# Optimization experiments

Measured on AMD Instinct MI355X. Metric: run time of the kernel, lower is better.

## Reference

```python
import jax, jax.numpy as jnp
import numpy as np
from jax import lax

# Dense-equivalent of the spconv net: SubMConv/SparseConv with stride 1 and
# size-preserving padding on a dense input reduce to ordinary conv2d.
# Layer chain: (1->64,k1) PReLU (64->256,k3) PReLU (256->512,k3) PReLU
# (512->256,k3) PReLU (256->64,k3) PReLU (64->1,k3) PReLU, then symmetrize.

CHANS = [(1, 64, 1), (64, 256, 3), (256, 512, 3), (512, 256, 3), (256, 64, 3), (64, 1, 3)]


def _conv(x, w, b, k):
    pad = ((k // 2, k // 2), (k // 2, k // 2))
    y = lax.conv_general_dilated(x, w, window_strides=(1, 1), padding=pad,
                                 dimension_numbers=('NCHW', 'OIHW', 'NCHW'))
    return y + b[None, :, None, None]


def _prelu(x, a):
    return jnp.where(x >= 0, x, a * x)


def setup_inputs() -> dict:
    key = jax.random.key(0)
    keys = jax.random.split(key, 1 + 2 * len(CHANS))
    inp = {'A': jax.random.normal(keys[0], (1, 1, 512, 512), dtype=jnp.float32)}
    for i, (cin, cout, k) in enumerate(CHANS):
        fan_in = cin * k * k
        std = 1.0 / np.sqrt(fan_in)
        inp[f'w{i}'] = jax.random.normal(keys[1 + 2 * i], (cout, cin, k, k), dtype=jnp.float32) * std
        inp[f'b{i}'] = jax.random.normal(keys[2 + 2 * i], (cout,), dtype=jnp.float32) * std
        inp[f'p{i}'] = jnp.full((1,), 0.25, dtype=jnp.float32)  # PReLU default weight
    return inp


def reference(A, w0, b0, p0, w1, b1, p1, w2, b2, p2, w3, b3, p3, w4, b4, p4, w5, b5, p5):
    params = [(w0, b0, p0), (w1, b1, p1), (w2, b2, p2), (w3, b3, p3), (w4, b4, p4), (w5, b5, p5)]
    x = A
    for (w, b, p), (_, _, k) in zip(params, CHANS):
        x = _prelu(_conv(x, w, b, k), p)
    # make_symmetric: average with transpose over the spatial (matrix) dims
    return 0.5 * (x + jnp.swapaxes(x, -1, -2))
```

## Files before the change

### kernel.cpp

```cpp
#include <hip/hip_runtime.h>
#include <hip/hip_bf16.h>
#include <stdint.h>

typedef __bf16 bf16_t;
typedef __bf16 bf16x8 __attribute__((ext_vector_type(8)));
typedef float  f32x4  __attribute__((ext_vector_type(4)));

#define HP 514
#define AS1 __attribute__((address_space(1)))
#define AS3 __attribute__((address_space(3)))

__device__ __forceinline__ bf16_t f2bf(float f) { return (bf16_t)f; }

__global__ void l0_kernel(const float* __restrict__ A, const float* __restrict__ w0,
                          const float* __restrict__ b0, const float* __restrict__ p0,
                          bf16_t* __restrict__ X0)
{
    int idx = blockIdx.x * 256 + threadIdx.x;
    if (idx >= HP * HP * 64) return;
    int c   = idx & 63;
    int pix = idx >> 6;
    int py = pix / HP, px = pix - py * HP;
    float v = 0.f;
    if (py >= 1 && py <= 512 && px >= 1 && px <= 512) {
        float a = A[(py - 1) * 512 + (px - 1)];
        v = fmaf(w0[c], a, b0[c]);
        v = v >= 0.f ? v : p0[0] * v;
    }
    X0[idx] = f2bf(v);
}

__global__ void zero_rows_kernel(bf16_t* __restrict__ buf, int C, int r0, int n)
{
    int idx = blockIdx.x * 256 + threadIdx.x;
    int rowsz = HP * C;
    if (idx >= n * rowsz) return;
    int r = idx / rowsz, j = idx - r * rowsz;
    buf[(size_t)(r0 + r) * rowsz + j] = f2bf(0.f);
}

__global__ void zero_cols_kernel(bf16_t* __restrict__ buf, int C, int R)
{
    int idx = blockIdx.x * 256 + threadIdx.x;
    if (idx >= R * 2 * C) return;
    int r = idx / (2 * C);
    int t = idx - r * 2 * C;
    int col = (t < C) ? 0 : 513;
    int c = t % C;
    buf[((size_t)r * HP + col) * C + c] = f2bf(0.f);
}

__global__ void wtrans_kernel(const float* __restrict__ w, bf16_t* __restrict__ wt,
                              int COUT, int CIN)
{
    int idx = blockIdx.x * 256 + threadIdx.x;
    if (idx >= COUT * CIN * 9) return;
    int G    = COUT / 16;
    int j    = idx & 7;
    int l    = (idx >> 3) & 63;
    int t    = idx >> 9;
    int gabs = t % G;
    int t2   = t / G;
    int tap  = t2 % 9;
    int ci   = t2 / 9;
    int cout = gabs * 16 + (l & 15);
    int cin  = ci * 32 + (l >> 4) * 8 + j;
    wt[idx] = f2bf(w[(cout * CIN + cin) * 9 + tap]);
}

template<int CIN, int COUT, int BN>
__global__ __launch_bounds__(256, 2)
void conv3x3_kernel(const bf16_t* __restrict__ in, const bf16_t* __restrict__ wt,
                    const float* __restrict__ bias, const float* __restrict__ alpha,
                    bf16_t* __restrict__ out,
                    int n_rows, int in_off, int in_alloc, int out_off)
{
    constexpr int G      = COUT / 16;
    constexpr int GPB    = BN / 16;
    constexpr int NT     = BN / 32;
    constexpr int NC     = CIN / 32;
    constexpr int AUNITS = 18 * 10 * 4;
    constexpr int ASLAB  = AUNITS * 8;
    constexpr int BSZ    = BN * 32;
    __shared__ __align__(16) bf16_t As[2 * ASLAB];
    __shared__ __align__(16) bf16_t Bs[2 * BSZ];

    const int tid  = threadIdx.x;
    const int lane = tid & 63;
    const int wave = tid >> 6;
    const int lm   = lane & 15;
    const int quad = lane >> 4;
    const int wave_m = wave >> 1;
    const int wave_n = wave & 1;

    const int x0 = blockIdx.x * 8;
    const int y0 = blockIdx.y * 16;
    const int zb = blockIdx.z;
    const int gb_blk = zb * GPB;

    int a_src[3], a_dst[3];
    #pragma unroll
    for (int it = 0; it < 3; ++it) {
        int u  = it * 256 + tid;
        int uu = u < AUNITS ? u : 0;
        int q = uu & 3, px = (uu >> 2) % 10, r = uu / 40;
        int grow = in_off + y0 + r;
        grow = grow < 0 ? 0 : (grow >= in_alloc ? in_alloc - 1 : grow);
        a_src[it] = (grow * HP + x0 + px) * CIN + q * 8;
        a_dst[it] = (r * 40 + px * 4 + ((q + (px >> 1)) & 3)) * 8;
    }

    const int pxb = lm & 7, pyb = lm >> 3;
    int sw[3];
    #pragma unroll
    for (int dx = 0; dx < 3; ++dx)
        sw[dx] = ((quad + ((pxb + dx) >> 1)) & 3) * 8;
    int addrA0[4];
    #pragma unroll
    for (int mt = 0; mt < 4; ++mt)
        addrA0[mt] = ((wave_m * 8 + mt * 2 + pyb) * 40 + pxb * 4) * 8;

    auto loadA = [&](int cc, bf16x8* s) {
        #pragma unroll
        for (int it = 0; it < 3; ++it)
            if (it * 256 + tid < AUNITS)
                s[it] = *(const bf16x8*)(in + a_src[it] + cc);
    };
    auto writeA = [&](const bf16x8* s, int abuf) {
        bf16_t* d = As + abuf * ASLAB;
        #pragma unroll
        for (int it = 0; it < 3; ++it)
            if (it * 256 + tid < AUNITS)
                *(bf16x8*)(d + a_dst[it]) = s[it];
    };
    auto stageB = [&](int ci9t, int bbuf) {
        #pragma unroll
        for (int k = 0; k < GPB / 4; ++k) {
            int g = wave + k * 4;
            const bf16_t* src = wt + ((size_t)ci9t * G + gb_blk + g) * 512 + lane * 8;
            bf16_t* dst = Bs + bbuf * BSZ + g * 512;
            __builtin_amdgcn_global_load_lds((AS1 void*)src, (AS3 void*)dst, 16, 0, 0);
        }
    };

    f32x4 acc[4][NT] = {};
    bf16x8 areg[3];

    loadA(0, areg);
    writeA(areg, 0);
    stageB(0, 0);
    __syncthreads();

    int ab = 0, bb = 0;
    for (int ci = 0; ci < NC; ++ci) {
        const bool more = (ci + 1 < NC);
        #pragma unroll
        for (int tap = 0; tap < 9; ++tap) {
            if (tap < 8)      stageB(ci * 9 + tap + 1, bb ^ 1);
            else if (more)    stageB((ci + 1) * 9, bb ^ 1);
            if (tap == 0 && more) loadA((ci + 1) * 32, areg);

            const int dy = tap / 3, dx = tap - dy * 3;
            const int shift = (dy * 40 + dx * 4) * 8 + sw[dx];
            bf16x8 a[4], b[NT];
            #pragma unroll
            for (int nt = 0; nt < NT; ++nt)
                b[nt] = *(const bf16x8*)(Bs + bb * BSZ + (wave_n * NT + nt) * 512 + lane * 8);
            #pragma unroll
            for (int mt = 0; mt < 4; ++mt)
                a[mt] = *(const bf16x8*)(As + ab * ASLAB + addrA0[mt] + shift);
            #pragma unroll
            for (int mt = 0; mt < 4; ++mt)
                #pragma unroll
                for (int nt = 0; nt < NT; ++nt)
                    acc[mt][nt] = __builtin_amdgcn_mfma_f32_16x16x32_bf16(
                        a[mt], b[nt], acc[mt][nt], 0, 0, 0);

            if (tap == 8 && more) writeA(areg, ab ^ 1);
            __syncthreads();
            bb ^= 1;
        }
        ab ^= 1;
    }

    const float al = alpha[0];
    #pragma unroll
    for (int nt = 0; nt < NT; ++nt) {
        const int n = zb * BN + wave_n * (BN / 2) + nt * 16 + lm;
        const float bv = bias[n];
        #pragma unroll
        for (int mt = 0; mt < 4; ++mt) {
            f32x4 v = acc[mt][nt];
            #pragma unroll
            for (int r = 0; r < 4; ++r) {
                int m  = wave_m * 64 + mt * 16 + quad * 4 + r;
                int py = m >> 3, px = m & 7;
                int ly = y0 + py;
                if (ly < n_rows) {
                    float f = v[r] + bv;
                    f = f >= 0.f ? f : al * f;
                    out[((size_t)(out_off + ly) * HP + (x0 + px + 1)) * COUT + n] = f2bf(f);
                }
            }
        }
    }
}

__device__ __forceinline__ float conv64_at(const bf16_t* __restrict__ X,
                                           const float* __restrict__ wsh,
                                           int y, int x, float bv)
{
    float acc = bv;
    #pragma unroll
    for (int dy = 0; dy < 3; ++dy) {
        #pragma unroll
        for (int dx = 0; dx < 3; ++dx) {
            const bf16x8* p = (const bf16x8*)(X + ((size_t)(y + dy) * HP + (x + dx)) * 64);
            const float* wf = wsh + (dy * 3 + dx) * 64;
            #pragma unroll
            for (int j = 0; j < 8; ++j) {
                bf16x8 v = p[j];
                #pragma unroll
                for (int k = 0; k < 8; ++k)
                    acc = fmaf((float)v[k], wf[j * 8 + k], acc);
            }
        }
    }
    return acc;
}

__global__ __launch_bounds__(256)
void l5_strip_kernel(const bf16_t* __restrict__ B4, const bf16_t* __restrict__ wt5,
                     const float* __restrict__ b5, const float* __restrict__ p5,
                     float* __restrict__ T, int abs_row0)
{
    __shared__ float wsh[9 * 64];
    for (int i = threadIdx.x; i < 576; i += 256) wsh[i] = (float)wt5[i];
    __syncthreads();
    int idx = blockIdx.x * 256 + threadIdx.x;
    int ly = idx >> 9, x = idx & 511;
    float bv = b5[0], al = p5[0];
    float t = conv64_at(B4, wsh, ly, x, bv);
    t = t >= 0.f ? t : al * t;
    T[(size_t)(abs_row0 + ly) * 512 + x] = t;
}

__global__ void wtrans5_kernel(const float* __restrict__ w, bf16_t* __restrict__ wt)
{
    int idx = blockIdx.x * 256 + threadIdx.x;
    if (idx >= 9 * 64) return;
    int cin = idx % 64, tap = idx / 64;
    wt[idx] = f2bf(w[cin * 9 + tap]);
}

__global__ __launch_bounds__(256)
void sym_kernel(const float* __restrict__ T, float* __restrict__ out)
{
    int idx = blockIdx.x * 256 + threadIdx.x;
    int y = idx >> 9, x = idx & 511;
    out[idx] = 0.5f * (T[idx] + T[x * 512 + y]);
}

extern "C" void kernel_launch(void* const* d_in, const int* in_sizes, int n_in,
                              void* d_out, int out_size, void* d_ws, size_t ws_size,
                              hipStream_t stream)
{
    const float* A = (const float*)d_in[0];
    const float *w[6], *b[6], *p[6];
    for (int i = 0; i < 6; ++i) {
        w[i] = (const float*)d_in[1 + 3 * i];
        b[i] = (const float*)d_in[2 + 3 * i];
        p[i] = (const float*)d_in[3 + 3 * i];
    }

    auto footprint = [](long long S) -> size_t {
        auto al = [](size_t v) { return (v + 255) & ~(size_t)255; };
        size_t t = 0;
        t += al((size_t)HP * HP * 64 * 2);
        t += al((size_t)(S + 8) * HP * 256 * 2);
        t += al((size_t)(S + 6) * HP * 512 * 2);
        t += al((size_t)(S + 2) * HP * 64 * 2);
        t += al((size_t)512 * 512 * 4);
        t += al((size_t)9 * 256 * 64 * 2);
        t += al((size_t)9 * 512 * 256 * 2);
        t += al((size_t)9 * 256 * 512 * 2);
        t += al((size_t)9 * 64 * 256 * 2);
        t += al((size_t)9 * 64 * 2);
        return t;
    };
    const int cand[6] = {512, 256, 128, 64, 32, 16};
    int S = 16;
    for (int i = 0; i < 6; ++i)
        if (footprint(cand[i]) <= ws_size) { S = cand[i]; break; }
    const int nStrips = 512 / S;

    char* ws = (char*)d_ws;
    size_t off = 0;
    auto carve = [&](size_t bytes) -> void* {
        void* r = ws + off;
        off += (bytes + 255) & ~(size_t)255;
        return r;
    };
    bf16_t* X0  = (bf16_t*)carve((size_t)HP * HP * 64 * 2);
    bf16_t* B1  = (bf16_t*)carve((size_t)(S + 8) * HP * 256 * 2);
    bf16_t* B2  = (bf16_t*)carve((size_t)(S + 6) * HP * 512 * 2);
    bf16_t* B4  = (bf16_t*)carve((size_t)(S + 2) * HP * 64 * 2);
    float*  T   = (float*)carve((size_t)512 * 512 * 4);
    bf16_t* wt1 = (bf16_t*)carve((size_t)9 * 256 * 64 * 2);
    bf16_t* wt2 = (bf16_t*)carve((size_t)9 * 512 * 256 * 2);
    bf16_t* wt3 = (bf16_t*)carve((size_t)9 * 256 * 512 * 2);
    bf16_t* wt4 = (bf16_t*)carve((size_t)9 * 64 * 256 * 2);
    bf16_t* wt5 = (bf16_t*)carve((size_t)9 * 64 * 2);
    bf16_t* B3  = B1;

    auto cdiv = [](int a, int bq) { return (a + bq - 1) / bq; };
    auto zrows = [&](bf16_t* buf, int C, int r0, int n) {
        if (n > 0)
            zero_rows_kernel<<<cdiv(n * HP * C, 256), 256, 0, stream>>>(buf, C, r0, n);
    };

    wtrans_kernel<<<cdiv(9 * 256 * 64, 256), 256, 0, stream>>>(w[1], wt1, 256, 64);
    wtrans_kernel<<<cdiv(9 * 512 * 256, 256), 256, 0, stream>>>(w[2], wt2, 512, 256);
    wtrans_kernel<<<cdiv(9 * 256 * 512, 256), 256, 0, stream>>>(w[3], wt3, 256, 512);
    wtrans_kernel<<<cdiv(9 * 64 * 256, 256), 256, 0, stream>>>(w[4], wt4, 64, 256);
    wtrans5_kernel<<<cdiv(9 * 64, 256), 256, 0, stream>>>(w[5], wt5);
    l0_kernel<<<cdiv(HP * HP * 64, 256), 256, 0, stream>>>(A, w[0], b[0], p[0], X0);
    zero_cols_kernel<<<cdiv((S + 8) * 2 * 256, 256), 256, 0, stream>>>(B1, 256, S + 8);
    zero_cols_kernel<<<cdiv((S + 6) * 2 * 512, 256), 256, 0, stream>>>(B2, 512, S + 6);
    zero_cols_kernel<<<cdiv((S + 2) * 2 * 64, 256), 256, 0, stream>>>(B4, 64, S + 2);

    for (int s = 0; s < nStrips; ++s) {
        const int base = S * s;
        int o0[5], nn[5], ooff[5], alloc[5];
        for (int k = 1; k <= 4; ++k) {
            int hk = 5 - k;
            int a0 = base - hk, a1 = base + S + hk;
            int c0 = a0 < 0 ? 0 : a0, c1 = a1 > 512 ? 512 : a1;
            o0[k] = c0; nn[k] = c1 - c0; ooff[k] = c0 - a0; alloc[k] = S + 2 * hk;
        }
        {
            int in_off = o0[1];
            dim3 g(64, cdiv(nn[1], 16), 2);
            conv3x3_kernel<64, 256, 128><<<g, 256, 0, stream>>>(
                X0, wt1, b[1], p[1], B1, nn[1], in_off, 514, ooff[1]);
            zrows(B1, 256, 0, ooff[1]);
            zrows(B1, 256, ooff[1] + nn[1], alloc[1] - ooff[1] - nn[1]);
        }
        {
            int in_off = (o0[2] - 1) - (base - 4);
            dim3 g(64, cdiv(nn[2], 16), 4);
            conv3x3_kernel<256, 512, 128><<<g, 256, 0, stream>>>(
                B1, wt2, b[2], p[2], B2, nn[2], in_off, alloc[1], ooff[2]);
            zrows(B2, 512, 0, ooff[2]);
            zrows(B2, 512, ooff[2] + nn[2], alloc[2] - ooff[2] - nn[2]);
        }
        {
            int in_off = (o0[3] - 1) - (base - 3);
            dim3 g(64, cdiv(nn[3], 16), 2);
            conv3x3_kernel<512, 256, 128><<<g, 256, 0, stream>>>(
                B2, wt3, b[3], p[3], B3, nn[3], in_off, alloc[2], ooff[3]);
            zrows(B3, 256, 0, ooff[3]);
            zrows(B3, 256, ooff[3] + nn[3], alloc[3] - ooff[3] - nn[3]);
        }
        {
            int in_off = (o0[4] - 1) - (base - 2);
            dim3 g(64, cdiv(nn[4], 16), 1);
            conv3x3_kernel<256, 64, 64><<<g, 256, 0, stream>>>(
                B3, wt4, b[4], p[4], B4, nn[4], in_off, alloc[3], ooff[4]);
            zrows(B4, 64, 0, ooff[4]);
            zrows(B4, 64, ooff[4] + nn[4], alloc[4] - ooff[4] - nn[4]);
        }
        l5_strip_kernel<<<(S * 512) / 256, 256, 0, stream>>>(B4, wt5, b[5], p[5], T, base);
    }

    sym_kernel<<<(512 * 512) / 256, 256, 0, stream>>>(T, (float*)d_out);
}
```

Before: 1.680 ms.

## Enlarge conv3x3 spatial tile to 16x16 and flatten grid with cout-fastest ordering

Doubles each block's spatial tile from 16x8 to 16x16 pixels, so each wave now computes 8 M-tiles instead of 4. The input halo overhead per output pixel drops and each B-fragment load feeds twice as many MFMAs. The 3D grid becomes a 1D grid in which the cout-block index varies fastest, so blocks sharing the same input tile run close together and can reuse it through the cache. In exchange the accumulators double (8xNT f32x4) and LDS use grows, which raises register pressure and may cut occupancy under launch_bounds(256,2).

```diff
diff --git a/kernel.cpp b/kernel.cpp
--- a/kernel.cpp
+++ b/kernel.cpp
@@ -77,10 +77,12 @@
 {
     constexpr int G      = COUT / 16;
     constexpr int GPB    = BN / 16;
-    constexpr int NT     = BN / 32;
+    constexpr int NT     = GPB / 2;
     constexpr int NC     = CIN / 32;
-    constexpr int AUNITS = 18 * 10 * 4;
-    constexpr int ASLAB  = AUNITS * 8;
+    constexpr int Z      = COUT / BN;
+    constexpr int AUNITS = 18 * 72;
+    constexpr int AROW   = 80;
+    constexpr int ASLAB  = 18 * AROW * 8;
     constexpr int BSZ    = BN * 32;
     __shared__ __align__(16) bf16_t As[2 * ASLAB];
     __shared__ __align__(16) bf16_t Bs[2 * BSZ];
@@ -93,58 +95,66 @@
     const int wave_m = wave >> 1;
     const int wave_n = wave & 1;
 
-    const int x0 = blockIdx.x * 8;
-    const int y0 = blockIdx.y * 16;
-    const int zb = blockIdx.z;
+    const int bid = blockIdx.x;
+    const int zb  = bid % Z;
+    const int tb  = bid / Z;
+    const int x0  = (tb & 31) * 16;
+    const int y0  = (tb >> 5) * 16;
     const int gb_blk = zb * GPB;
 
-    int a_src[3], a_dst[3];
-    #pragma unroll
-    for (int it = 0; it < 3; ++it) {
+    int a_src[6], a_dst[6];
+    #pragma unroll
+    for (int it = 0; it < 6; ++it) {
         int u  = it * 256 + tid;
         int uu = u < AUNITS ? u : 0;
-        int q = uu & 3, px = (uu >> 2) % 10, r = uu / 40;
+        int r = uu / 72, rem = uu - r * 72;
+        int px = rem >> 2, q = rem & 3;
         int grow = in_off + y0 + r;
         grow = grow < 0 ? 0 : (grow >= in_alloc ? in_alloc - 1 : grow);
         a_src[it] = (grow * HP + x0 + px) * CIN + q * 8;
-        a_dst[it] = (r * 40 + px * 4 + ((q + (px >> 1)) & 3)) * 8;
-    }
-
-    const int pxb = lm & 7, pyb = lm >> 3;
+        a_dst[it] = (r * AROW + px * 4 + ((q + (px >> 1)) & 3)) * 8;
+    }
+    const bool tail_ok = (tid < 16);
+
+    const int pxl = lm & 7, pyl = lm >> 3;
     int sw[3];
     #pragma unroll
     for (int dx = 0; dx < 3; ++dx)
-        sw[dx] = ((quad + ((pxb + dx) >> 1)) & 3) * 8;
-    int addrA0[4];
-    #pragma unroll
-    for (int mt = 0; mt < 4; ++mt)
-        addrA0[mt] = ((wave_m * 8 + mt * 2 + pyb) * 40 + pxb * 4) * 8;
+        sw[dx] = ((quad + ((pxl + dx) >> 1)) & 3) * 8;
+    int addrA0[8];
+    #pragma unroll
+    for (int mt = 0; mt < 8; ++mt) {
+        int ry = mt >> 1, rx = mt & 1;
+        int row0 = (wave_m * 4 + ry) * 2 + pyl;
+        int px0  = rx * 8 + pxl;
+        addrA0[mt] = (row0 * AROW + px0 * 4) * 8;
+    }
 
     auto loadA = [&](int cc, bf16x8* s) {
         #pragma unroll
-        for (int it = 0; it < 3; ++it)
-            if (it * 256 + tid < AUNITS)
-                s[it] = *(const bf16x8*)(in + a_src[it] + cc);
+        for (int it = 0; it < 5; ++it) s[it] = *(const bf16x8*)(in + a_src[it] + cc);
+        if (tail_ok) s[5] = *(const bf16x8*)(in + a_src[5] + cc);
     };
     auto writeA = [&](const bf16x8* s, int abuf) {
         bf16_t* d = As + abuf * ASLAB;
         #pragma unroll
-        for (int it = 0; it < 3; ++it)
-            if (it * 256 + tid < AUNITS)
-                *(bf16x8*)(d + a_dst[it]) = s[it];
+        for (int it = 0; it < 5; ++it) *(bf16x8*)(d + a_dst[it]) = s[it];
+        if (tail_ok) *(bf16x8*)(d + a_dst[5]) = s[5];
     };
     auto stageB = [&](int ci9t, int bbuf) {
         #pragma unroll
-        for (int k = 0; k < GPB / 4; ++k) {
+        for (int k = 0; k < (GPB + 3) / 4; ++k) {
             int g = wave + k * 4;
-            const bf16_t* src = wt + ((size_t)ci9t * G + gb_blk + g) * 512 + lane * 8;
-            bf16_t* dst = Bs + bbuf * BSZ + g * 512;
-            __builtin_amdgcn_global_load_lds((AS1 void*)src, (AS3 void*)dst, 16, 0, 0);
-        }
-    };
-
-    f32x4 acc[4][NT] = {};
-    bf16x8 areg[3];
+            if (g < GPB) {
+                const bf16_t* src = wt + ((size_t)ci9t * G + gb_blk + g) * 512 + lane * 8;
+                bf16_t* dst = Bs + bbuf * BSZ + g * 512;
+                __builtin_amdgcn_global_load_lds((AS1 void*)src, (AS3 void*)dst, 16, 0, 0);
+            }
+        }
+    };
+
+    f32x4 acc[8][NT] = {};
+    bf16x8 areg[6];
 
     loadA(0, areg);
     writeA(areg, 0);
@@ -161,20 +171,24 @@
             if (tap == 0 && more) loadA((ci + 1) * 32, areg);
 
             const int dy = tap / 3, dx = tap - dy * 3;
-            const int shift = (dy * 40 + dx * 4) * 8 + sw[dx];
-            bf16x8 a[4], b[NT];
+            const int shift = (dy * AROW + dx * 4) * 8 + sw[dx];
+            bf16x8 b[NT];
             #pragma unroll
             for (int nt = 0; nt < NT; ++nt)
                 b[nt] = *(const bf16x8*)(Bs + bb * BSZ + (wave_n * NT + nt) * 512 + lane * 8);
             #pragma unroll
-            for (int mt = 0; mt < 4; ++mt)
-                a[mt] = *(const bf16x8*)(As + ab * ASLAB + addrA0[mt] + shift);
-            #pragma unroll
-            for (int mt = 0; mt < 4; ++mt)
+            for (int h = 0; h < 2; ++h) {
+                bf16x8 a[4];
                 #pragma unroll
-                for (int nt = 0; nt < NT; ++nt)
-                    acc[mt][nt] = __builtin_amdgcn_mfma_f32_16x16x32_bf16(
-                        a[mt], b[nt], acc[mt][nt], 0, 0, 0);
+                for (int j = 0; j < 4; ++j)
+                    a[j] = *(const bf16x8*)(As + ab * ASLAB + addrA0[h * 4 + j] + shift);
+                #pragma unroll
+                for (int j = 0; j < 4; ++j)
+                    #pragma unroll
+                    for (int nt = 0; nt < NT; ++nt)
+                        acc[h * 4 + j][nt] = __builtin_amdgcn_mfma_f32_16x16x32_bf16(
+                            a[j], b[nt], acc[h * 4 + j][nt], 0, 0, 0);
+            }
 
             if (tap == 8 && more) writeA(areg, ab ^ 1);
             __syncthreads();
@@ -186,15 +200,17 @@
     const float al = alpha[0];
     #pragma unroll
     for (int nt = 0; nt < NT; ++nt) {
-        const int n = zb * BN + wave_n * (BN / 2) + nt * 16 + lm;
+        const int n = zb * BN + (wave_n * NT + nt) * 16 + lm;
         const float bv = bias[n];
         #pragma unroll
-        for (int mt = 0; mt < 4; ++mt) {
+        for (int mt = 0; mt < 8; ++mt) {
+            const int ry = mt >> 1, rx = mt & 1;
             f32x4 v = acc[mt][nt];
             #pragma unroll
             for (int r = 0; r < 4; ++r) {
-                int m  = wave_m * 64 + mt * 16 + quad * 4 + r;
-                int py = m >> 3, px = m & 7;
+                int i  = quad * 4 + r;
+                int py = (wave_m * 4 + ry) * 2 + (i >> 3);
+                int px = rx * 8 + (i & 7);
                 int ly = y0 + py;
                 if (ly < n_rows) {
                     float f = v[r] + bv;
@@ -340,32 +356,28 @@
         }
         {
             int in_off = o0[1];
-            dim3 g(64, cdiv(nn[1], 16), 2);
-            conv3x3_kernel<64, 256, 128><<<g, 256, 0, stream>>>(
+            conv3x3_kernel<64, 256, 128><<<dim3(32 * cdiv(nn[1], 16) * 2), 256, 0, stream>>>(
                 X0, wt1, b[1], p[1], B1, nn[1], in_off, 514, ooff[1]);
             zrows(B1, 256, 0, ooff[1]);
             zrows(B1, 256, ooff[1] + nn[1], alloc[1] - ooff[1] - nn[1]);
         }
         {
             int in_off = (o0[2] - 1) - (base - 4);
-            dim3 g(64, cdiv(nn[2], 16), 4);
-            conv3x3_kernel<256, 512, 128><<<g, 256, 0, stream>>>(
+            conv3x3_kernel<256, 512, 128><<<dim3(32 * cdiv(nn[2], 16) * 4), 256, 0, stream>>>(
                 B1, wt2, b[2], p[2], B2, nn[2], in_off, alloc[1], ooff[2]);
             zrows(B2, 512, 0, ooff[2]);
             zrows(B2, 512, ooff[2] + nn[2], alloc[2] - ooff[2] - nn[2]);
         }
         {
             int in_off = (o0[3] - 1) - (base - 3);
-            dim3 g(64, cdiv(nn[3], 16), 2);
-            conv3x3_kernel<512, 256, 128><<<g, 256, 0, stream>>>(
+            conv3x3_kernel<512, 256, 128><<<dim3(32 * cdiv(nn[3], 16) * 2), 256, 0, stream>>>(
                 B2, wt3, b[3], p[3], B3, nn[3], in_off, alloc[2], ooff[3]);
             zrows(B3, 256, 0, ooff[3]);
             zrows(B3, 256, ooff[3] + nn[3], alloc[3] - ooff[3] - nn[3]);
         }
         {
             int in_off = (o0[4] - 1) - (base - 2);
-            dim3 g(64, cdiv(nn[4], 16), 1);
-            conv3x3_kernel<256, 64, 64><<<g, 256, 0, stream>>>(
+            conv3x3_kernel<256, 64, 64><<<dim3(32 * cdiv(nn[4], 16) * 1), 256, 0, stream>>>(
                 B3, wt4, b[4], p[4], B4, nn[4], in_off, alloc[3], ooff[4]);
             zrows(B4, 64, 0, ooff[4]);
             zrows(B4, 64, ooff[4] + nn[4], alloc[4] - ooff[4] - nn[4]);
```

New measurement: 2.144 ms. +27.6%, slower.
